# Optimization experiments

Measured on AMD Instinct MI355X. Metric: run time of the kernel, lower is better.

The kernel has to match this reference:

```python
import jax, jax.numpy as jnp
import numpy as np
from jax import lax


def setup_inputs() -> dict:
    key = jax.random.key(0)
    kx, kw = jax.random.split(key)
    x = jax.random.normal(kx, (32, 3, 8192), dtype=jnp.float32)
    weight = jax.random.normal(kw, (128, 3, 64), dtype=jnp.float32)
    return {"x": x, "weight": weight}


def reference(x, weight):
    # x: [B, C, L], weight: [O, C, K]
    K = weight.shape[2]
    # Cross-correlation (conv1d, no bias, valid padding): [B, O, L-K+1]
    conv_out = lax.conv_general_dilated(
        x, weight, window_strides=(1,), padding='VALID',
        dimension_numbers=('NCH', 'OIH', 'NCH'))
    # Half squared norm of each shapelet: [O]
    w_norm = jnp.sum(weight ** 2, axis=(1, 2)) / 2
    # Half squared norm of each length-K window, via cumulative sums
    # (avoids materializing the [B, C, W, K] unfold tensor)
    sq = jnp.sum(x ** 2, axis=1)               # [B, L]
    c = jnp.pad(jnp.cumsum(sq, axis=1), ((0, 0), (1, 0)))  # [B, L+1]
    win_norm = (c[:, K:] - c[:, :-K]) / 2      # [B, L-K+1]
    # features = conv_out - (||w||^2/2 + ||window||^2/2)
    features = conv_out - w_norm[None, :, None] - win_norm[:, None, :]
    # global max-pool over time, then *(-2) -> min squared distance
    return -2.0 * jnp.max(features, axis=-1)   # [B, O]
```

## Files before the change

### kernel.cpp

```cpp
#include <hip/hip_runtime.h>
#include <float.h>

#define BB 32
#define LL 8192
#define OO 128
#define KK 64
#define WW (LL - KK + 1)
#define TC 32

typedef __attribute__((ext_vector_type(8))) short short8;
typedef __attribute__((ext_vector_type(4))) float f32x4;

union AB { int4 i4; int i[4]; short8 v; };

static __device__ __forceinline__ unsigned int f2bf(float f) {
    unsigned int u = __builtin_bit_cast(unsigned int, f);
    return (u + 0x7FFFu + ((u >> 16) & 1u)) >> 16;
}

__global__ __launch_bounds__(256, 4) void shapeconv_main(const float* __restrict__ x,
                                                         const float* __restrict__ w,
                                                         float* __restrict__ partial) {
    __shared__ __align__(16) unsigned short w_lds[64 * 200];
    __shared__ __align__(16) unsigned short x_lds[3 * 320];
    __shared__ float sq_lds[320];
    __shared__ float P_lds[40];
    __shared__ float win_lds[272];
    __shared__ float wn_lds[64];
    __shared__ float mred[64];

    const int tc = blockIdx.x;
    const int ob = blockIdx.y;
    const int b  = blockIdx.z;
    const int tid = threadIdx.x;
    const int wv = tid >> 6;
    const int lane = tid & 63;
    const int wo = wv & 1, wt = wv >> 1;
    const int n  = lane & 15;
    const int qp = lane >> 4;
    const int T0 = tc * 256;

    {
        int o = tid >> 2, q = tid & 3;
        const float4* p = (const float4*)(w + (ob * 64 + o) * 192 + q * 48);
        unsigned short* dst = w_lds + o * 200 + q * 48;
        float s = 0.f;
        #pragma unroll
        for (int i = 0; i < 6; ++i) {
            float4 v0 = p[2 * i], v1 = p[2 * i + 1];
            s = fmaf(v0.x, v0.x, s); s = fmaf(v0.y, v0.y, s);
            s = fmaf(v0.z, v0.z, s); s = fmaf(v0.w, v0.w, s);
            s = fmaf(v1.x, v1.x, s); s = fmaf(v1.y, v1.y, s);
            s = fmaf(v1.z, v1.z, s); s = fmaf(v1.w, v1.w, s);
            int4 pk;
            pk.x = (int)(f2bf(v0.x) | (f2bf(v0.y) << 16));
            pk.y = (int)(f2bf(v0.z) | (f2bf(v0.w) << 16));
            pk.z = (int)(f2bf(v1.x) | (f2bf(v1.y) << 16));
            pk.w = (int)(f2bf(v1.z) | (f2bf(v1.w) << 16));
            *(int4*)(dst + 8 * i) = pk;
        }
        s += __shfl_xor(s, 1, 64);
        s += __shfl_xor(s, 2, 64);
        if (q == 0) wn_lds[o] = 0.5f * s;
    }

    {
        int i = tid;
        if (i < 240) {
            int c = i / 80, j4 = i - c * 80;
            int l = T0 + j4 * 4;
            float4 v = make_float4(0.f, 0.f, 0.f, 0.f);
            if (l < LL) v = *(const float4*)(x + (b * 3 + c) * LL + l);
            uint2 pk;
            pk.x = f2bf(v.x) | (f2bf(v.y) << 16);
            pk.y = f2bf(v.z) | (f2bf(v.w) << 16);
            *(uint2*)(x_lds + c * 320 + j4 * 4) = pk;
        }
    }
    for (int j = tid; j < 320; j += 256) {
        int l = T0 + j;
        float s = 0.f;
        if (l < LL) {
            #pragma unroll
            for (int c = 0; c < 3; ++c) {
                float v = x[(b * 3 + c) * LL + l];
                s = fmaf(v, v, s);
            }
        }
        sq_lds[j] = s;
    }
    if (tid < 40) {
        float s = 0.f;
        #pragma unroll
        for (int k = 0; k < 8; ++k) {
            int l = T0 + tid * 8 + k;
            if (l < LL) {
                #pragma unroll
                for (int c = 0; c < 3; ++c) {
                    float v = x[(b * 3 + c) * LL + l];
                    s = fmaf(v, v, s);
                }
            }
        }
        P_lds[tid] = s;
    }
    __syncthreads();

    {
        int a = tid >> 3, bb2 = tid & 7;
        float s = 0.f;
        #pragma unroll
        for (int i = 1; i <= 7; ++i) s += P_lds[a + i];
        #pragma unroll
        for (int k = 0; k < 8; ++k)
            s += (k >= bb2) ? sq_lds[8 * a + k] : sq_lds[8 * a + 64 + k];
        int pi = tid + (tid >> 4);
        win_lds[pi] = (T0 + tid < WW) ? 0.5f * s : 1e30f;
    }
    __syncthreads();

    f32x4 acc[2][8];
    {
        float wl[8];
        #pragma unroll
        for (int r = 0; r < 8; ++r) {
            int tl = 128 * wt + r + 8 * n;
            wl[r] = win_lds[tl + (tl >> 4)];
        }
        #pragma unroll
        for (int ot = 0; ot < 2; ++ot)
            #pragma unroll
            for (int rg = 0; rg < 4; ++rg) {
                float nw = wn_lds[32 * wo + 16 * ot + 4 * qp + rg];
                #pragma unroll
                for (int r = 0; r < 8; ++r)
                    acc[ot][r][rg] = -nw - wl[r];
            }
    }

    const char* xb = (const char*)x_lds;
    const char* wb = (const char*)w_lds;
    #pragma unroll
    for (int ks = 0; ks < 6; ++ks) {
        int c = ks >> 1, h = ks & 1;
        int e0b = c * 640 + 256 * wt + 64 * h + 16 * (n + qp);
        int4 Ea = *(const int4*)(xb + e0b);
        int4 Eb = *(const int4*)(xb + e0b + 16);
        int D[8] = {Ea.x, Ea.y, Ea.z, Ea.w, Eb.x, Eb.y, Eb.z, Eb.w};
        AB a0, a1;
        int ab0 = (32 * wo + n) * 400 + 128 * c + 64 * h + 16 * qp;
        a0.i4 = *(const int4*)(wb + ab0);
        a1.i4 = *(const int4*)(wb + ab0 + 16 * 400);
        #pragma unroll
        for (int r = 0; r < 8; ++r) {
            AB bf;
            int s = r >> 1;
            if ((r & 1) == 0) {
                bf.i[0] = D[s]; bf.i[1] = D[s + 1]; bf.i[2] = D[s + 2]; bf.i[3] = D[s + 3];
            } else {
                #pragma unroll
                for (int d = 0; d < 4; ++d)
                    bf.i[d] = (int)(((unsigned)D[s + d] >> 16) | ((unsigned)D[s + d + 1] << 16));
            }
            acc[0][r] = __builtin_amdgcn_mfma_f32_16x16x32_bf16(a0.v, bf.v, acc[0][r], 0, 0, 0);
            acc[1][r] = __builtin_amdgcn_mfma_f32_16x16x32_bf16(a1.v, bf.v, acc[1][r], 0, 0, 0);
        }
    }

    float m2[2][4];
    #pragma unroll
    for (int ot = 0; ot < 2; ++ot)
        #pragma unroll
        for (int rg = 0; rg < 4; ++rg) {
            float mm = acc[ot][0][rg];
            #pragma unroll
            for (int r = 1; r < 8; ++r) mm = fmaxf(mm, acc[ot][r][rg]);
            m2[ot][rg] = mm;
        }
    #pragma unroll
    for (int s = 1; s <= 8; s <<= 1)
        #pragma unroll
        for (int ot = 0; ot < 2; ++ot)
            #pragma unroll
            for (int rg = 0; rg < 4; ++rg)
                m2[ot][rg] = fmaxf(m2[ot][rg], __shfl_xor(m2[ot][rg], s, 64));

    if (wt == 1 && n == 0) {
        #pragma unroll
        for (int ot = 0; ot < 2; ++ot)
            #pragma unroll
            for (int rg = 0; rg < 4; ++rg)
                mred[32 * wo + 16 * ot + 4 * qp + rg] = m2[ot][rg];
    }
    __syncthreads();
    if (wt == 0 && n == 0) {
        #pragma unroll
        for (int ot = 0; ot < 2; ++ot)
            #pragma unroll
            for (int rg = 0; rg < 4; ++rg) {
                int oi = 32 * wo + 16 * ot + 4 * qp + rg;
                float v = fmaxf(m2[ot][rg], mred[oi]);
                partial[((size_t)(b * TC + tc) * 2 + ob) * 64 + oi] = v;
            }
    }
}

__global__ __launch_bounds__(256) void reduce_kernel(const float* __restrict__ partial,
                                                     float* __restrict__ out) {
    int idx = blockIdx.x * 256 + threadIdx.x;
    int b = idx >> 7, o = idx & 127;
    const float* pp = partial + ((size_t)b * TC * 2 + (o >> 6)) * 64 + (o & 63);
    float mx = -FLT_MAX;
    #pragma unroll 8
    for (int tcc = 0; tcc < TC; ++tcc) mx = fmaxf(mx, pp[(size_t)tcc * 128]);
    out[idx] = -2.f * mx;
}

extern "C" void kernel_launch(void* const* d_in, const int* in_sizes, int n_in,
                              void* d_out, int out_size, void* d_ws, size_t ws_size,
                              hipStream_t stream) {
    const float* x = (const float*)d_in[0];
    const float* w = (const float*)d_in[1];
    float* out = (float*)d_out;
    float* partial = (float*)d_ws;

    dim3 grid(TC, 2, BB);
    shapeconv_main<<<grid, 256, 0, stream>>>(x, w, partial);
    reduce_kernel<<<16, 256, 0, stream>>>(partial, out);
}
```

Measured before the change: 82.23 us.

## Precompute bf16 swizzled weights and norms in a prep kernel

Adds a small prep kernel that converts the weights to bf16 once, stores them in an MFMA-friendly swizzled order, and computes the half squared norms. The main kernel then copies the pre-swizzled weights straight into LDS with coalesced int4 copies instead of converting and reducing per block, and reads A fragments with a simpler contiguous pattern. This removes redundant per-block conversion work across 2048 blocks and shrinks LDS use, at the cost of one extra kernel launch and a global round trip for the weights.

```diff
diff --git a/kernel.cpp b/kernel.cpp
--- a/kernel.cpp
+++ b/kernel.cpp
@@ -18,10 +18,40 @@
     return (u + 0x7FFFu + ((u >> 16) & 1u)) >> 16;
 }
 
+__global__ __launch_bounds__(256) void prep_kernel(const float* __restrict__ w,
+                                                   unsigned short* __restrict__ wswz,
+                                                   float* __restrict__ wn) {
+    int g = blockIdx.x * 256 + threadIdx.x;
+    if (g < 3072) {
+        int ob = (g >= 1536) ? 1 : 0;
+        int gg = g - ob * 1536;
+        int ksqp = gg >> 6;
+        int o2   = gg & 63;
+        int ks = ksqp >> 2, qp = ksqp & 3;
+        int c = ks >> 1, h = ks & 1;
+        const float4* p = (const float4*)(w + (ob * 64 + o2) * 192 + c * 64 + h * 32 + qp * 8);
+        float4 v0 = p[0], v1 = p[1];
+        int4 pk;
+        pk.x = (int)(f2bf(v0.x) | (f2bf(v0.y) << 16));
+        pk.y = (int)(f2bf(v0.z) | (f2bf(v0.w) << 16));
+        pk.z = (int)(f2bf(v1.x) | (f2bf(v1.y) << 16));
+        pk.w = (int)(f2bf(v1.z) | (f2bf(v1.w) << 16));
+        ((int4*)wswz)[g] = pk;
+    }
+    int oo = g - 3072;
+    if (oo >= 0 && oo < OO) {
+        const float* p = w + oo * 192;
+        float s = 0.f;
+        for (int i = 0; i < 192; ++i) { float v = p[i]; s = fmaf(v, v, s); }
+        wn[oo] = 0.5f * s;
+    }
+}
+
 __global__ __launch_bounds__(256, 4) void shapeconv_main(const float* __restrict__ x,
-                                                         const float* __restrict__ w,
+                                                         const unsigned short* __restrict__ wswz,
+                                                         const float* __restrict__ wn,
                                                          float* __restrict__ partial) {
-    __shared__ __align__(16) unsigned short w_lds[64 * 200];
+    __shared__ __align__(16) unsigned short w_lds[64 * 192];
     __shared__ __align__(16) unsigned short x_lds[3 * 320];
     __shared__ float sq_lds[320];
     __shared__ float P_lds[40];
@@ -41,41 +71,23 @@
     const int T0 = tc * 256;
 
     {
-        int o = tid >> 2, q = tid & 3;
-        const float4* p = (const float4*)(w + (ob * 64 + o) * 192 + q * 48);
-        unsigned short* dst = w_lds + o * 200 + q * 48;
-        float s = 0.f;
-        #pragma unroll
-        for (int i = 0; i < 6; ++i) {
-            float4 v0 = p[2 * i], v1 = p[2 * i + 1];
-            s = fmaf(v0.x, v0.x, s); s = fmaf(v0.y, v0.y, s);
-            s = fmaf(v0.z, v0.z, s); s = fmaf(v0.w, v0.w, s);
-            s = fmaf(v1.x, v1.x, s); s = fmaf(v1.y, v1.y, s);
-            s = fmaf(v1.z, v1.z, s); s = fmaf(v1.w, v1.w, s);
-            int4 pk;
-            pk.x = (int)(f2bf(v0.x) | (f2bf(v0.y) << 16));
-            pk.y = (int)(f2bf(v0.z) | (f2bf(v0.w) << 16));
-            pk.z = (int)(f2bf(v1.x) | (f2bf(v1.y) << 16));
-            pk.w = (int)(f2bf(v1.z) | (f2bf(v1.w) << 16));
-            *(int4*)(dst + 8 * i) = pk;
-        }
-        s += __shfl_xor(s, 1, 64);
-        s += __shfl_xor(s, 2, 64);
-        if (q == 0) wn_lds[o] = 0.5f * s;
-    }
-
-    {
-        int i = tid;
-        if (i < 240) {
-            int c = i / 80, j4 = i - c * 80;
-            int l = T0 + j4 * 4;
-            float4 v = make_float4(0.f, 0.f, 0.f, 0.f);
-            if (l < LL) v = *(const float4*)(x + (b * 3 + c) * LL + l);
-            uint2 pk;
-            pk.x = f2bf(v.x) | (f2bf(v.y) << 16);
-            pk.y = f2bf(v.z) | (f2bf(v.w) << 16);
-            *(uint2*)(x_lds + c * 320 + j4 * 4) = pk;
-        }
+        const int4* src = (const int4*)wswz + ob * 1536;
+        int4* dst = (int4*)w_lds;
+        #pragma unroll
+        for (int i = 0; i < 6; ++i)
+            dst[tid + 256 * i] = src[tid + 256 * i];
+    }
+    if (tid < 64) wn_lds[tid] = wn[ob * 64 + tid];
+
+    if (tid < 240) {
+        int c = tid / 80, j4 = tid - c * 80;
+        int l = T0 + j4 * 4;
+        float4 v = make_float4(0.f, 0.f, 0.f, 0.f);
+        if (l < LL) v = *(const float4*)(x + (b * 3 + c) * LL + l);
+        uint2 pk;
+        pk.x = f2bf(v.x) | (f2bf(v.y) << 16);
+        pk.y = f2bf(v.z) | (f2bf(v.w) << 16);
+        *(uint2*)(x_lds + c * 320 + j4 * 4) = pk;
     }
     for (int j = tid; j < 320; j += 256) {
         int l = T0 + j;
@@ -139,7 +151,6 @@
     }
 
     const char* xb = (const char*)x_lds;
-    const char* wb = (const char*)w_lds;
     #pragma unroll
     for (int ks = 0; ks < 6; ++ks) {
         int c = ks >> 1, h = ks & 1;
@@ -148,9 +159,9 @@
         int4 Eb = *(const int4*)(xb + e0b + 16);
         int D[8] = {Ea.x, Ea.y, Ea.z, Ea.w, Eb.x, Eb.y, Eb.z, Eb.w};
         AB a0, a1;
-        int ab0 = (32 * wo + n) * 400 + 128 * c + 64 * h + 16 * qp;
-        a0.i4 = *(const int4*)(wb + ab0);
-        a1.i4 = *(const int4*)(wb + ab0 + 16 * 400);
+        const int4* wq = (const int4*)w_lds + (ks * 4 + qp) * 64 + 32 * wo;
+        a0.i4 = wq[n];
+        a1.i4 = wq[16 + n];
         #pragma unroll
         for (int r = 0; r < 8; ++r) {
             AB bf;
@@ -222,9 +233,13 @@
     const float* x = (const float*)d_in[0];
     const float* w = (const float*)d_in[1];
     float* out = (float*)d_out;
-    float* partial = (float*)d_ws;
-
+
+    unsigned short* wswz = (unsigned short*)d_ws;
+    float* wn = (float*)((char*)d_ws + 49152);
+    float* partial = (float*)((char*)d_ws + 49664);
+
+    prep_kernel<<<13, 256, 0, stream>>>(w, wswz, wn);
     dim3 grid(TC, 2, BB);
-    shapeconv_main<<<grid, 256, 0, stream>>>(x, w, partial);
+    shapeconv_main<<<grid, 256, 0, stream>>>(x, wswz, wn, partial);
     reduce_kernel<<<16, 256, 0, stream>>>(partial, out);
 }
```

Result: no change. 83.83 us (+1.9%).
